# Kernel optimization log

Hardware: AMD Instinct MI355X
Metric: run time of the kernel (lower is better)

## Reference

```python
import jax, jax.numpy as jnp
import numpy as np

S = 32            # state: nodes per graph, conv output channels
B = 4096          # number of graphs
N = B * S         # total nodes
E = 2 * 1024 * 1024  # total edges (avg degree 16)
A = 2             # action_space_dimension
NACT = 32         # number_of_actions (adv heads)
EPS = 1e-5


def setup_inputs() -> dict:
    key = jax.random.key(0)
    ks = jax.random.split(key, 24)
    f = lambda k, sh, s: (jax.random.normal(k, sh, jnp.float32) * s)
    return {
        'x': f(ks[0], (N, 2), 1.0),
        'edge_index': jax.random.randint(ks[1], (2, E), 0, N),
        # conv1 MLP: Linear(4,16) -> ReLU -> Linear(16,S)
        'c1W1': f(ks[2], (4, 16), 0.5), 'c1b1': jnp.zeros((16,), jnp.float32),
        'c1W2': f(ks[3], (16, S), 0.25), 'c1b2': jnp.zeros((S,), jnp.float32),
        # conv2/conv3 MLPs: Linear(2*S,16) -> ReLU -> Linear(16,S)
        'c2W1': f(ks[4], (2 * S, 16), 0.12), 'c2b1': jnp.zeros((16,), jnp.float32),
        'c2W2': f(ks[5], (16, S), 0.25), 'c2b2': jnp.zeros((S,), jnp.float32),
        'c3W1': f(ks[6], (2 * S, 16), 0.12), 'c3b1': jnp.zeros((16,), jnp.float32),
        'c3W2': f(ks[7], (16, S), 0.25), 'c3b2': jnp.zeros((S,), jnp.float32),
        # 3 BatchNorm1d(S) layers (stacked)
        'bn_g': jnp.ones((3, S), jnp.float32), 'bn_b': jnp.zeros((3, S), jnp.float32),
        # dense head MLP 1024->256->256->256
        'mW1': f(ks[8], (S * S, 256), 0.03), 'mb1': jnp.zeros((256,), jnp.float32),
        'mW2': f(ks[9], (256, 256), 0.06), 'mb2': jnp.zeros((256,), jnp.float32),
        'mW3': f(ks[10], (256, 256), 0.06), 'mb3': jnp.zeros((256,), jnp.float32),
        # dueling heads
        'vW': f(ks[11], (256, 1), 0.06), 'vb': jnp.zeros((1,), jnp.float32),
        'aW': f(ks[12], (NACT, 256, A), 0.06), 'ab': jnp.zeros((NACT, A), jnp.float32),
    }


def _edgeconv(x, src, dst, W1, b1, W2, b2):
    # PyG EdgeConv with aggr='add': msg = MLP(cat[x_i, x_j - x_i]), summed at target i
    xi = x[dst]                       # [E, F]
    xj = x[src]                       # [E, F]
    m = jnp.concatenate([xi, xj - xi], axis=-1)        # [E, 2F]
    h = jnp.maximum(m @ W1 + b1, 0.0) @ W2 + b2        # [E, S]
    return jax.ops.segment_sum(h, dst, num_segments=x.shape[0])  # [N, S]


def _bn(h, g, b):
    # BatchNorm1d in training mode: batch stats over node dim, biased variance
    mu = h.mean(axis=0)
    var = jnp.mean((h - mu) ** 2, axis=0)
    return (h - mu) * jax.lax.rsqrt(var + EPS) * g + b


def reference(x, edge_index, c1W1, c1b1, c1W2, c1b2, c2W1, c2b1, c2W2, c2b2,
              c3W1, c3b1, c3W2, c3b2, bn_g, bn_b, mW1, mb1, mW2, mb2,
              mW3, mb3, vW, vb, aW, ab):
    src, dst = edge_index[0], edge_index[1]
    h = _edgeconv(x, src, dst, c1W1, c1b1, c1W2, c1b2)
    h = jax.nn.relu(_bn(h, bn_g[0], bn_b[0]))
    h = _edgeconv(h, src, dst, c2W1, c2b1, c2W2, c2b2)
    h = jax.nn.relu(_bn(h, bn_g[1], bn_b[1]))
    h = _edgeconv(h, src, dst, c3W1, c3b1, c3W2, c3b2)
    h = jax.nn.relu(_bn(h, bn_g[2], bn_b[2]))
    nb = x.shape[0] // S                                 # graphs in batch
    out = h.reshape(nb, S * S)                           # [B, in_size]
    out = jax.nn.relu(out @ mW1 + mb1)
    out = jax.nn.relu(out @ mW2 + mb2)
    out = jax.nn.relu(out @ mW3 + mb3)                   # [B, 256]
    value = out @ vW + vb                                # [B, 1]
    adv = jnp.einsum('bf,nfa->bna', out, aW) + ab        # [B, NACT, A]
    q = value[:, :, None] + adv - adv.mean(axis=2, keepdims=True)
    return q
```

## Files before the change

### kernel.cpp

```cpp
#include <hip/hip_runtime.h>
#include <hip/hip_fp16.h>

#define NN 131072
#define EE 2097152
#define SS 32
#define HH 16
#define BB 4096
#define EPS 1e-5f

#define BKT 512
#define BNODES 256
#define CAP 4864
#define SCAP 8192
#define TILE 8192

typedef _Float16 f16x8 __attribute__((ext_vector_type(8)));
typedef float f32x4 __attribute__((ext_vector_type(4)));

__global__ __launch_bounds__(1024) void k_bsort(const int* __restrict__ ei, int* __restrict__ gcount,
                                                int* __restrict__ words) {
    __shared__ int cnt[BKT];
    __shared__ int tstart[BKT];
    __shared__ int gshift[BKT];
    __shared__ int sc[BKT];
    __shared__ int sword[TILE];
    __shared__ int sdst[TILE];
    int t = threadIdx.x;
    if (t < BKT) cnt[t] = 0;
    __syncthreads();
    int e0 = blockIdx.x * TILE;
#pragma unroll
    for (int it = 0; it < TILE / 1024; ++it) {
        int dst = ei[EE + e0 + it * 1024 + t];
        atomicAdd(&cnt[dst >> 8], 1);
    }
    __syncthreads();
    int val = (t < BKT) ? cnt[t] : 0;
    if (t < BKT) sc[t] = val;
    __syncthreads();
    for (int d = 1; d < BKT; d <<= 1) {
        int v2 = (t >= d && t < BKT) ? sc[t - d] : 0;
        __syncthreads();
        if (t < BKT) sc[t] += v2;
        __syncthreads();
    }
    if (t < BKT) {
        int excl = sc[t] - val;
        tstart[t] = excl;
        gshift[t] = t * CAP + atomicAdd(&gcount[t], val) - excl;
        cnt[t] = 0;
    }
    __syncthreads();
#pragma unroll
    for (int it = 0; it < TILE / 1024; ++it) {
        int e = e0 + it * 1024 + t;
        int src = ei[e];
        int dst = ei[EE + e];
        int b = dst >> 8;
        int r = atomicAdd(&cnt[b], 1);
        int p = tstart[b] + r;
        sword[p] = src | ((dst & 255) << 17);
        sdst[p] = gshift[b] + p;
    }
    __syncthreads();
#pragma unroll
    for (int it = 0; it < TILE / 1024; ++it) {
        int i = it * 1024 + t;
        words[sdst[i]] = sword[i];
    }
}

__global__ __launch_bounds__(512) void k_csr(const int* __restrict__ words, const int* __restrict__ gcount,
                                             int* __restrict__ ssrc, int* __restrict__ offs,
                                             int* __restrict__ offe) {
    __shared__ int hist[BNODES];
    __shared__ int sc[BNODES];
    __shared__ int base[BNODES];
    int t = threadIdx.x;
    int b = blockIdx.x;
    if (t < BNODES) hist[t] = 0;
    __syncthreads();
    int cnt = gcount[b];
    const int* wp = words + (size_t)b * CAP;
    for (int p = t; p < cnt; p += 512) atomicAdd(&hist[wp[p] >> 17], 1);
    __syncthreads();
    int val = 0, pval = 0;
    if (t < BNODES) {
        val = hist[t];
        pval = (val + 15) & ~15;
        sc[t] = pval;
    }
    __syncthreads();
    for (int d = 1; d < BNODES; d <<= 1) {
        int v2 = (t >= d && t < BNODES) ? sc[t - d] : 0;
        __syncthreads();
        if (t < BNODES) sc[t] += v2;
        __syncthreads();
    }
    int gbase = b * SCAP;
    if (t < BNODES) {
        base[t] = sc[t] - pval;
        offs[b * BNODES + t] = gbase + base[t];
        offe[b * BNODES + t] = gbase + base[t] + val;
        hist[t] = 0;
    }
    __syncthreads();
    for (int p = t; p < cnt; p += 512) {
        int w = wp[p];
        int dl = w >> 17;
        int r = atomicAdd(&hist[dl], 1);
        ssrc[gbase + base[dl] + r] = w & 0x1FFFF;
    }
    if (t < BNODES) {
        int s = gbase + base[t];
        for (int i = val; i < pval; ++i) ssrc[s + i] = NN;
    }
}

__global__ __launch_bounds__(256) void k_prep(const float* __restrict__ mW1, const float* __restrict__ mW2,
                                              const float* __restrict__ mW3, const float* __restrict__ vW,
                                              const float* __restrict__ vb, const float* __restrict__ aW,
                                              const float* __restrict__ ab,
                                              _Float16* __restrict__ W1T, _Float16* __restrict__ W2T,
                                              _Float16* __restrict__ W3T, _Float16* __restrict__ BqT,
                                              float* __restrict__ biasq, int* __restrict__ gcount,
                                              float* __restrict__ bns) {
    int i = blockIdx.x * 256 + threadIdx.x;
    {
        int k = i >> 8, n = i & 255;
        W1T[(size_t)n * 1024 + k] = (_Float16)mW1[i];
    }
    if (i < 65536) {
        int k = i >> 8, n = i & 255;
        W2T[n * 256 + k] = (_Float16)mW2[i];
        W3T[n * 256 + k] = (_Float16)mW3[i];
    }
    if (i < 16384) {
        int f = i >> 6, j = i & 63;
        int n = j >> 1, a = j & 1;
        float wa = aW[n * 512 + f * 2 + a];
        float wo = aW[n * 512 + f * 2 + (1 - a)];
        BqT[j * 256 + f] = (_Float16)(vW[f] + 0.5f * (wa - wo));
    }
    if (i < 64) biasq[i] = vb[0] + 0.5f * (ab[i] - ab[i ^ 1]);
    if (i < 512) gcount[i] = 0;
    if (i < 192) bns[i] = 0.f;
}

__global__ __launch_bounds__(256) void k_pre1(const float* __restrict__ x, const float* __restrict__ W1,
                                              const float* __restrict__ b1, float* __restrict__ u,
                                              __half* __restrict__ v) {
    int t = blockIdx.x * 256 + threadIdx.x;
    int n = t >> 4, c = t & 15;
    float x0 = x[n * 2], x1 = x[n * 2 + 1];
    float w0 = W1[c], w1 = W1[16 + c], w2 = W1[32 + c], w3 = W1[48 + c];
    u[t] = b1[c] + x0 * (w0 - w2) + x1 * (w1 - w3);
    v[t] = __float2half(x0 * w2 + x1 * w3);
    if (blockIdx.x == 0 && t < 16) v[NN * 16 + t] = __float2half(-60000.0f);
}

__global__ __launch_bounds__(256) void k_bnpre(const float* __restrict__ y, const float* __restrict__ bns,
                                               const float* __restrict__ g, const float* __restrict__ bb,
                                               const float* __restrict__ W1, const float* __restrict__ b1,
                                               float* __restrict__ u, __half* __restrict__ v) {
    __shared__ float sh[16][33];
    __shared__ float wd[32][16];
    __shared__ float wv[32][16];
    __shared__ float scL[32], soL[32];
    int t = threadIdx.x;
    if (t < 32) {
        const float inv_n = 1.0f / (float)NN;
        float mean = bns[t] * inv_n;
        float var = bns[32 + t] * inv_n - mean * mean;
        float s = g[t] * rsqrtf(var + EPS);
        scL[t] = s;
        soL[t] = bb[t] - mean * s;
    }
    for (int i = t; i < 512; i += 256) {
        int f = i >> 4, c = i & 15;
        float wt = W1[i];
        float wb = W1[512 + i];
        wd[f][c] = wt - wb;
        wv[f][c] = wb;
    }
    __syncthreads();
    int nb = blockIdx.x * 16;
    for (int i = t; i < 512; i += 256) {
        int col = i & 31;
        sh[i >> 5][col] = fmaxf(y[nb * 32 + i] * scL[col] + soL[col], 0.f);
    }
    __syncthreads();
    int c = t & 15, nl = t >> 4;
    float uu = b1[c], vv = 0.f;
#pragma unroll
    for (int f = 0; f < 32; ++f) {
        float hv = sh[nl][f];
        uu += hv * wd[f][c];
        vv += hv * wv[f][c];
    }
    int n = nb + nl;
    u[n * 16 + c] = uu;
    v[n * 16 + c] = __float2half(vv);
    if (blockIdx.x == 0 && t < 16) v[NN * 16 + t] = __float2half(-60000.0f);
}

__global__ __launch_bounds__(256) void k_gather(const float* __restrict__ u, const __half* __restrict__ v,
                                                const int* __restrict__ ssrc, const int* __restrict__ offs,
                                                const int* __restrict__ offe,
                                                const float* __restrict__ W2, const float* __restrict__ b2,
                                                float* __restrict__ y) {
    __shared__ float sw2[512];
    __shared__ float sagg[32 * 18];
    __shared__ float cntL[32];
    int t = threadIdx.x;
    float w2a = W2[t], w2b = W2[t + 256];
    float b2r0 = b2[(t & 7) * 4], b2r1 = b2[(t & 7) * 4 + 1];
    float b2r2 = b2[(t & 7) * 4 + 2], b2r3 = b2[(t & 7) * 4 + 3];
    int nl = t >> 3, s = t & 7;
    int e2 = s >> 1;
    int h = s & 1;
    int n = blockIdx.x * 32 + nl;
    int s0 = offs[n], e0 = offe[n];
    int pe = s0 + ((e0 - s0 + 15) & ~15);
    float ur[8];
    *(float4*)&ur[0] = *(const float4*)(u + (size_t)n * 16 + h * 8);
    *(float4*)&ur[4] = *(const float4*)(u + (size_t)n * 16 + h * 8 + 4);
    float acc[8] = {};
    for (int p = s0; p < pe; p += 16) {
        int b0 = p + e2;
        int i0 = ssrc[b0], i1 = ssrc[b0 + 4], i2 = ssrc[b0 + 8], i3 = ssrc[b0 + 12];
        float4 r0 = ((const float4*)(v + (size_t)i0 * 16))[h];
        float4 r1 = ((const float4*)(v + (size_t)i1 * 16))[h];
        float4 r2 = ((const float4*)(v + (size_t)i2 * 16))[h];
        float4 r3 = ((const float4*)(v + (size_t)i3 * 16))[h];
        const float4* rs[4] = {&r0, &r1, &r2, &r3};
#pragma unroll
        for (int e = 0; e < 4; ++e) {
            const __half2* hp = (const __half2*)rs[e];
#pragma unroll
            for (int k = 0; k < 4; ++k) {
                float2 f = __half22float2(hp[k]);
                acc[2 * k]     += fmaxf(ur[2 * k] + f.x, 0.f);
                acc[2 * k + 1] += fmaxf(ur[2 * k + 1] + f.y, 0.f);
            }
        }
    }
#pragma unroll
    for (int j = 0; j < 8; ++j) {
        acc[j] += __shfl_xor(acc[j], 2);
        acc[j] += __shfl_xor(acc[j], 4);
    }
    if (e2 == 0) {
#pragma unroll
        for (int j = 0; j < 8; ++j) sagg[nl * 18 + h * 8 + j] = acc[j];
    }
    if (s == 0) cntL[nl] = (float)(e0 - s0);
    sw2[t] = w2a;
    sw2[t + 256] = w2b;
    __syncthreads();
    int node = t >> 3, oc = (t & 7) * 4;
    float cw = cntL[node];
    float o0 = b2r0 * cw, o1 = b2r1 * cw, o2 = b2r2 * cw, o3 = b2r3 * cw;
#pragma unroll
    for (int k = 0; k < 16; ++k) {
        float a = sagg[node * 18 + k];
        o0 += a * sw2[k * 32 + oc];
        o1 += a * sw2[k * 32 + oc + 1];
        o2 += a * sw2[k * 32 + oc + 2];
        o3 += a * sw2[k * 32 + oc + 3];
    }
    *(float4*)(y + (size_t)(blockIdx.x * 32 + node) * 32 + oc) = make_float4(o0, o1, o2, o3);
}

__global__ __launch_bounds__(256) void k_bnstat2(const float* __restrict__ y, float* __restrict__ bns) {
    __shared__ float ssm[8][33];
    __shared__ float ssq[8][33];
    int t = threadIdx.x;
    int c = t & 31, g = t >> 5;
    size_t r0 = (size_t)blockIdx.x * 512;
    float sm = 0.f, sq = 0.f;
    for (int i = 0; i < 64; ++i) {
        float val = y[(r0 + g + (size_t)i * 8) * 32 + c];
        sm += val;
        sq += val * val;
    }
    ssm[g][c] = sm;
    ssq[g][c] = sq;
    __syncthreads();
    if (t < 32) {
        float a = 0.f, bq = 0.f;
#pragma unroll
        for (int gg = 0; gg < 8; ++gg) { a += ssm[gg][t]; bq += ssq[gg][t]; }
        atomicAdd(&bns[t], a);
        atomicAdd(&bns[32 + t], bq);
    }
}

__global__ __launch_bounds__(256) void k_bnrelu16(const float* __restrict__ y, const float* __restrict__ bns,
                                                  const float* __restrict__ g, const float* __restrict__ bb,
                                                  _Float16* __restrict__ h16) {
    int t = blockIdx.x * 256 + threadIdx.x;
    int j = t & 31;
    const float inv_n = 1.0f / (float)NN;
    float mean = bns[j] * inv_n;
    float var = bns[32 + j] * inv_n - mean * mean;
    float sc = g[j] * rsqrtf(var + EPS);
    float sh = bb[j] - mean * sc;
    h16[t] = (_Float16)fmaxf(y[t] * sc + sh, 0.f);
}

__global__ __launch_bounds__(256) void k_mgemm(const _Float16* __restrict__ A, const _Float16* __restrict__ BT,
                                               const float* __restrict__ bias, float* __restrict__ Cf,
                                               _Float16* __restrict__ Ch, int M, int N, int K,
                                               int relu, int out16) {
    int tid = threadIdx.x;
    int w = tid >> 6, l = tid & 63, q = l >> 4, r = l & 15;
    int rowBase = blockIdx.x * 64;
    int col = blockIdx.y * 64 + w * 16 + r;
    const _Float16* ap = A + (size_t)(rowBase + r) * K + q * 8;
    const _Float16* bp = BT + (size_t)col * K + q * 8;
    f32x4 z = {0.f, 0.f, 0.f, 0.f};
    f32x4 acc[4] = {z, z, z, z};
    for (int k0 = 0; k0 < K; k0 += 32) {
        f16x8 bf = *(const f16x8*)(bp + k0);
        f16x8 a0 = *(const f16x8*)(ap + k0);
        f16x8 a1 = *(const f16x8*)(ap + k0 + (size_t)16 * K);
        f16x8 a2 = *(const f16x8*)(ap + k0 + (size_t)32 * K);
        f16x8 a3 = *(const f16x8*)(ap + k0 + (size_t)48 * K);
        acc[0] = __builtin_amdgcn_mfma_f32_16x16x32_f16(a0, bf, acc[0], 0, 0, 0);
        acc[1] = __builtin_amdgcn_mfma_f32_16x16x32_f16(a1, bf, acc[1], 0, 0, 0);
        acc[2] = __builtin_amdgcn_mfma_f32_16x16x32_f16(a2, bf, acc[2], 0, 0, 0);
        acc[3] = __builtin_amdgcn_mfma_f32_16x16x32_f16(a3, bf, acc[3], 0, 0, 0);
    }
    float bv = bias[col];
#pragma unroll
    for (int rt = 0; rt < 4; ++rt) {
#pragma unroll
        for (int i = 0; i < 4; ++i) {
            int row = rowBase + rt * 16 + q * 4 + i;
            float val = acc[rt][i] + bv;
            if (relu) val = fmaxf(val, 0.f);
            if (out16) Ch[(size_t)row * N + col] = (_Float16)val;
            else       Cf[(size_t)row * N + col] = val;
        }
    }
}

extern "C" void kernel_launch(void* const* d_in, const int* in_sizes, int n_in,
                              void* d_out, int out_size, void* d_ws, size_t ws_size,
                              hipStream_t stream) {
    const float* x    = (const float*)d_in[0];
    const int*   ei   = (const int*)d_in[1];
    const float* c1W1 = (const float*)d_in[2];
    const float* c1b1 = (const float*)d_in[3];
    const float* c1W2 = (const float*)d_in[4];
    const float* c1b2 = (const float*)d_in[5];
    const float* c2W1 = (const float*)d_in[6];
    const float* c2b1 = (const float*)d_in[7];
    const float* c2W2 = (const float*)d_in[8];
    const float* c2b2 = (const float*)d_in[9];
    const float* c3W1 = (const float*)d_in[10];
    const float* c3b1 = (const float*)d_in[11];
    const float* c3W2 = (const float*)d_in[12];
    const float* c3b2 = (const float*)d_in[13];
    const float* bn_g = (const float*)d_in[14];
    const float* bn_b = (const float*)d_in[15];
    const float* mW1  = (const float*)d_in[16];
    const float* mb1  = (const float*)d_in[17];
    const float* mW2  = (const float*)d_in[18];
    const float* mb2  = (const float*)d_in[19];
    const float* mW3  = (const float*)d_in[20];
    const float* mb3  = (const float*)d_in[21];
    const float* vW   = (const float*)d_in[22];
    const float* vb   = (const float*)d_in[23];
    const float* aW   = (const float*)d_in[24];
    const float* ab   = (const float*)d_in[25];
    float* out = (float*)d_out;

    char* p = (char*)d_ws;
    auto take = [&](size_t bytes) {
        char* r = p;
        p += (bytes + 255) & ~(size_t)255;
        return r;
    };
    int*       gcount = (int*)take((size_t)BKT * 4);
    int*       words  = (int*)take((size_t)BKT * CAP * 4);
    int*       ssrc   = (int*)take((size_t)BKT * SCAP * 4);
    int*       offs   = (int*)take((size_t)NN * 4);
    int*       offe   = (int*)take((size_t)NN * 4);
    float*     u      = (float*)take((size_t)NN * HH * 4);
    __half*    v      = (__half*)take((size_t)(NN + 1) * HH * 2);
    float*     y      = (float*)take((size_t)NN * SS * 4);
    _Float16*  h16    = (_Float16*)take((size_t)NN * SS * 2);
    float*     bns    = (float*)take(3 * 64 * 4);
    _Float16*  W1T    = (_Float16*)take((size_t)256 * 1024 * 2);
    _Float16*  W2T    = (_Float16*)take((size_t)256 * 256 * 2);
    _Float16*  W3T    = (_Float16*)take((size_t)256 * 256 * 2);
    _Float16*  BqT    = (_Float16*)take((size_t)64 * 256 * 2);
    float*     biasq  = (float*)take(64 * 4);
    _Float16*  Xa     = (_Float16*)take((size_t)BB * 256 * 2);
    _Float16*  Xb     = (_Float16*)take((size_t)BB * 256 * 2);

    k_prep<<<1024, 256, 0, stream>>>(mW1, mW2, mW3, vW, vb, aW, ab,
                                     W1T, W2T, W3T, BqT, biasq, gcount, bns);

    k_bsort<<<EE / TILE, 1024, 0, stream>>>(ei, gcount, words);
    k_csr<<<BKT, 512, 0, stream>>>(words, gcount, ssrc, offs, offe);

    k_pre1<<<NN * 16 / 256, 256, 0, stream>>>(x, c1W1, c1b1, u, v);
    k_gather<<<NN / 32, 256, 0, stream>>>(u, v, ssrc, offs, offe, c1W2, c1b2, y);
    k_bnstat2<<<256, 256, 0, stream>>>(y, bns);
    k_bnpre<<<NN / 16, 256, 0, stream>>>(y, bns, bn_g, bn_b, c2W1, c2b1, u, v);
    k_gather<<<NN / 32, 256, 0, stream>>>(u, v, ssrc, offs, offe, c2W2, c2b2, y);
    k_bnstat2<<<256, 256, 0, stream>>>(y, bns + 64);
    k_bnpre<<<NN / 16, 256, 0, stream>>>(y, bns + 64, bn_g + 32, bn_b + 32, c3W1, c3b1, u, v);
    k_gather<<<NN / 32, 256, 0, stream>>>(u, v, ssrc, offs, offe, c3W2, c3b2, y);
    k_bnstat2<<<256, 256, 0, stream>>>(y, bns + 128);
    k_bnrelu16<<<NN * 32 / 256, 256, 0, stream>>>(y, bns + 128, bn_g + 64, bn_b + 64, h16);

    k_mgemm<<<dim3(BB / 64, 4), 256, 0, stream>>>(h16, W1T, mb1, nullptr, Xa, BB, 256, 1024, 1, 1);
    k_mgemm<<<dim3(BB / 64, 4), 256, 0, stream>>>(Xa, W2T, mb2, nullptr, Xb, BB, 256, 256, 1, 1);
    k_mgemm<<<dim3(BB / 64, 4), 256, 0, stream>>>(Xb, W3T, mb3, nullptr, Xa, BB, 256, 256, 1, 1);
    k_mgemm<<<dim3(BB / 64, 1), 256, 0, stream>>>(Xa, BqT, biasq, out, nullptr, BB, 64, 256, 0, 0);
}
```

Measured before the change: 333.5 us.

## Fuse BN statistics into gather epilogue and merge layer-1 pre into prep

The gather kernel now accumulates per-channel sum and sum-of-squares in shared memory and writes per-block partials. A small deterministic reduction kernel replaces the separate stats pass, so y is no longer re-read for BN statistics. The layer-1 u/v precompute also moves into the prep kernel, which saves one launch; the prep grid grows to cover all nodes. The cost is extra shared-memory atomics in the gather epilogue and a partials buffer write.

```diff
diff --git a/kernel.cpp b/kernel.cpp
--- a/kernel.cpp
+++ b/kernel.cpp
@@ -117,16 +117,25 @@
     }
 }
 
-__global__ __launch_bounds__(256) void k_prep(const float* __restrict__ mW1, const float* __restrict__ mW2,
+__global__ __launch_bounds__(256) void k_prep(const float* __restrict__ x, const float* __restrict__ c1W1,
+                                              const float* __restrict__ c1b1,
+                                              const float* __restrict__ mW1, const float* __restrict__ mW2,
                                               const float* __restrict__ mW3, const float* __restrict__ vW,
                                               const float* __restrict__ vb, const float* __restrict__ aW,
                                               const float* __restrict__ ab,
+                                              float* __restrict__ u, __half* __restrict__ v,
                                               _Float16* __restrict__ W1T, _Float16* __restrict__ W2T,
                                               _Float16* __restrict__ W3T, _Float16* __restrict__ BqT,
-                                              float* __restrict__ biasq, int* __restrict__ gcount,
-                                              float* __restrict__ bns) {
+                                              float* __restrict__ biasq, int* __restrict__ gcount) {
     int i = blockIdx.x * 256 + threadIdx.x;
     {
+        int n = i >> 4, c = i & 15;
+        float x0 = x[n * 2], x1 = x[n * 2 + 1];
+        float w0 = c1W1[c], w1 = c1W1[16 + c], w2 = c1W1[32 + c], w3 = c1W1[48 + c];
+        u[i] = c1b1[c] + x0 * (w0 - w2) + x1 * (w1 - w3);
+        v[i] = __float2half(x0 * w2 + x1 * w3);
+    }
+    if (i < 262144) {
         int k = i >> 8, n = i & 255;
         W1T[(size_t)n * 1024 + k] = (_Float16)mW1[i];
     }
@@ -144,19 +153,7 @@
     }
     if (i < 64) biasq[i] = vb[0] + 0.5f * (ab[i] - ab[i ^ 1]);
     if (i < 512) gcount[i] = 0;
-    if (i < 192) bns[i] = 0.f;
-}
-
-__global__ __launch_bounds__(256) void k_pre1(const float* __restrict__ x, const float* __restrict__ W1,
-                                              const float* __restrict__ b1, float* __restrict__ u,
-                                              __half* __restrict__ v) {
-    int t = blockIdx.x * 256 + threadIdx.x;
-    int n = t >> 4, c = t & 15;
-    float x0 = x[n * 2], x1 = x[n * 2 + 1];
-    float w0 = W1[c], w1 = W1[16 + c], w2 = W1[32 + c], w3 = W1[48 + c];
-    u[t] = b1[c] + x0 * (w0 - w2) + x1 * (w1 - w3);
-    v[t] = __float2half(x0 * w2 + x1 * w3);
-    if (blockIdx.x == 0 && t < 16) v[NN * 16 + t] = __float2half(-60000.0f);
+    if (i < 16) v[NN * 16 + i] = __float2half(-60000.0f);
 }
 
 __global__ __launch_bounds__(256) void k_bnpre(const float* __restrict__ y, const float* __restrict__ bns,
@@ -208,11 +205,13 @@
                                                 const int* __restrict__ ssrc, const int* __restrict__ offs,
                                                 const int* __restrict__ offe,
                                                 const float* __restrict__ W2, const float* __restrict__ b2,
-                                                float* __restrict__ y) {
+                                                float* __restrict__ y, float* __restrict__ part) {
     __shared__ float sw2[512];
     __shared__ float sagg[32 * 18];
     __shared__ float cntL[32];
+    __shared__ float sbn[64];
     int t = threadIdx.x;
+    if (t < 64) sbn[t] = 0.f;
     float w2a = W2[t], w2b = W2[t + 256];
     float b2r0 = b2[(t & 7) * 4], b2r1 = b2[(t & 7) * 4 + 1];
     float b2r2 = b2[(t & 7) * 4 + 2], b2r3 = b2[(t & 7) * 4 + 3];
@@ -270,30 +269,31 @@
         o3 += a * sw2[k * 32 + oc + 3];
     }
     *(float4*)(y + (size_t)(blockIdx.x * 32 + node) * 32 + oc) = make_float4(o0, o1, o2, o3);
-}
-
-__global__ __launch_bounds__(256) void k_bnstat2(const float* __restrict__ y, float* __restrict__ bns) {
-    __shared__ float ssm[8][33];
-    __shared__ float ssq[8][33];
+    atomicAdd(&sbn[oc + 0], o0);
+    atomicAdd(&sbn[oc + 1], o1);
+    atomicAdd(&sbn[oc + 2], o2);
+    atomicAdd(&sbn[oc + 3], o3);
+    atomicAdd(&sbn[32 + oc + 0], o0 * o0);
+    atomicAdd(&sbn[32 + oc + 1], o1 * o1);
+    atomicAdd(&sbn[32 + oc + 2], o2 * o2);
+    atomicAdd(&sbn[32 + oc + 3], o3 * o3);
+    __syncthreads();
+    if (t < 64) part[(size_t)blockIdx.x * 64 + t] = sbn[t];
+}
+
+__global__ __launch_bounds__(256) void k_bnred(const float* __restrict__ part, float* __restrict__ bns) {
+    __shared__ float s[256];
+    int j = blockIdx.x;
     int t = threadIdx.x;
-    int c = t & 31, g = t >> 5;
-    size_t r0 = (size_t)blockIdx.x * 512;
-    float sm = 0.f, sq = 0.f;
-    for (int i = 0; i < 64; ++i) {
-        float val = y[(r0 + g + (size_t)i * 8) * 32 + c];
-        sm += val;
-        sq += val * val;
-    }
-    ssm[g][c] = sm;
-    ssq[g][c] = sq;
-    __syncthreads();
-    if (t < 32) {
-        float a = 0.f, bq = 0.f;
-#pragma unroll
-        for (int gg = 0; gg < 8; ++gg) { a += ssm[gg][t]; bq += ssq[gg][t]; }
-        atomicAdd(&bns[t], a);
-        atomicAdd(&bns[32 + t], bq);
-    }
+    float a = 0.f;
+    for (int b = t; b < NN / 32; b += 256) a += part[(size_t)b * 64 + j];
+    s[t] = a;
+    __syncthreads();
+    for (int d = 128; d > 0; d >>= 1) {
+        if (t < d) s[t] += s[t + d];
+        __syncthreads();
+    }
+    if (t == 0) bns[j] = s[0];
 }
 
 __global__ __launch_bounds__(256) void k_bnrelu16(const float* __restrict__ y, const float* __restrict__ bns,
@@ -393,6 +393,7 @@
     float*     y      = (float*)take((size_t)NN * SS * 4);
     _Float16*  h16    = (_Float16*)take((size_t)NN * SS * 2);
     float*     bns    = (float*)take(3 * 64 * 4);
+    float*     part   = (float*)take((size_t)(NN / 32) * 64 * 4);
     _Float16*  W1T    = (_Float16*)take((size_t)256 * 1024 * 2);
     _Float16*  W2T    = (_Float16*)take((size_t)256 * 256 * 2);
     _Float16*  W3T    = (_Float16*)take((size_t)256 * 256 * 2);
@@ -401,21 +402,20 @@
     _Float16*  Xa     = (_Float16*)take((size_t)BB * 256 * 2);
     _Float16*  Xb     = (_Float16*)take((size_t)BB * 256 * 2);
 
-    k_prep<<<1024, 256, 0, stream>>>(mW1, mW2, mW3, vW, vb, aW, ab,
-                                     W1T, W2T, W3T, BqT, biasq, gcount, bns);
+    k_prep<<<NN * 16 / 256, 256, 0, stream>>>(x, c1W1, c1b1, mW1, mW2, mW3, vW, vb, aW, ab,
+                                              u, v, W1T, W2T, W3T, BqT, biasq, gcount);
 
     k_bsort<<<EE / TILE, 1024, 0, stream>>>(ei, gcount, words);
     k_csr<<<BKT, 512, 0, stream>>>(words, gcount, ssrc, offs, offe);
 
-    k_pre1<<<NN * 16 / 256, 256, 0, stream>>>(x, c1W1, c1b1, u, v);
-    k_gather<<<NN / 32, 256, 0, stream>>>(u, v, ssrc, offs, offe, c1W2, c1b2, y);
-    k_bnstat2<<<256, 256, 0, stream>>>(y, bns);
+    k_gather<<<NN / 32, 256, 0, stream>>>(u, v, ssrc, offs, offe, c1W2, c1b2, y, part);
+    k_bnred<<<64, 256, 0, stream>>>(part, bns);
     k_bnpre<<<NN / 16, 256, 0, stream>>>(y, bns, bn_g, bn_b, c2W1, c2b1, u, v);
-    k_gather<<<NN / 32, 256, 0, stream>>>(u, v, ssrc, offs, offe, c2W2, c2b2, y);
-    k_bnstat2<<<256, 256, 0, stream>>>(y, bns + 64);
+    k_gather<<<NN / 32, 256, 0, stream>>>(u, v, ssrc, offs, offe, c2W2, c2b2, y, part);
+    k_bnred<<<64, 256, 0, stream>>>(part, bns + 64);
     k_bnpre<<<NN / 16, 256, 0, stream>>>(y, bns + 64, bn_g + 32, bn_b + 32, c3W1, c3b1, u, v);
-    k_gather<<<NN / 32, 256, 0, stream>>>(u, v, ssrc, offs, offe, c3W2, c3b2, y);
-    k_bnstat2<<<256, 256, 0, stream>>>(y, bns + 128);
+    k_gather<<<NN / 32, 256, 0, stream>>>(u, v, ssrc, offs, offe, c3W2, c3b2, y, part);
+    k_bnred<<<64, 256, 0, stream>>>(part, bns + 128);
     k_bnrelu16<<<NN * 32 / 256, 256, 0, stream>>>(y, bns + 128, bn_g + 64, bn_b + 64, h16);
 
     k_mgemm<<<dim3(BB / 64, 4), 256, 0, stream>>>(h16, W1T, mb1, nullptr, Xa, BB, 256, 1024, 1, 1);
```

Result: slower. 426.4 us (+27.9%).
